# Kernel tuning notes

Measured on AMD Instinct MI355X. Metric: run time of the kernel, lower is better.

The kernel has to match this reference:

```python
import jax, jax.numpy as jnp
import numpy as np

# dims (match init_kwargs)
V = 100000   # vocab_size
E = 512      # embedding_dim
HID = 1024   # hidden_dim (bi-LSTM output size)
H = HID // 2 # per-direction LSTM hidden
T = 32       # num_of_tag
S = 8192     # sequence length
START, STOP = 30, 31
NEG = -10000.0


def setup_inputs() -> dict:
    key = jax.random.key(0)
    ks = jax.random.split(key, 11)
    n = lambda k, shape, s=0.1: jax.random.normal(k, shape, dtype=jnp.float32) * s
    trans = jax.random.normal(ks[9], (T, T), dtype=jnp.float32)
    trans = trans.at[:, START].set(NEG)   # nothing transitions INTO start
    trans = trans.at[STOP, :].set(NEG)    # nothing transitions OUT of stop
    return {
        "inputs": jax.random.randint(ks[0], (S,), 0, V, dtype=jnp.int32),
        "embed": n(ks[1], (V, E), 1.0),
        "W_ih_f": n(ks[2], (4 * H, E)),
        "W_hh_f": n(ks[3], (4 * H, H)),
        "b_f": n(ks[4], (4 * H,)),        # b_ih + b_hh fused
        "W_ih_b": n(ks[5], (4 * H, E)),
        "W_hh_b": n(ks[6], (4 * H, H)),
        "b_b": n(ks[7], (4 * H,)),
        "fc_W": n(ks[8], (T, HID)),
        "fc_b": jnp.zeros((T,), jnp.float32),
        "trans": trans,
    }


def _lstm_dir(x, W_ih, W_hh, b):
    """Single-direction LSTM, PyTorch gate order (i, f, g, o). x: [S, E] -> [S, H]."""
    xp = x @ W_ih.T + b  # [S, 4H], precomputed input projections

    def step(carry, xp_t):
        h, c = carry
        gates = xp_t + h @ W_hh.T
        i, f, g, o = jnp.split(gates, 4)
        i, f, o = jax.nn.sigmoid(i), jax.nn.sigmoid(f), jax.nn.sigmoid(o)
        g = jnp.tanh(g)
        c = f * c + i * g
        h = o * jnp.tanh(c)
        return (h, c), h

    init = (jnp.zeros((H,), x.dtype), jnp.zeros((H,), x.dtype))
    _, hs = jax.lax.scan(step, init, xp)
    return hs


def _viterbi(feats, trans):
    """feats: [S, T]. Vectorized Viterbi DP over the TxT transition matrix."""
    init = jnp.full((T,), NEG, feats.dtype).at[START].set(0.0)

    def step(prev, feat):
        scores = prev[:, None] + trans          # [prev_tag, next_tag]
        bp = jnp.argmax(scores, axis=0)         # best previous tag per next tag
        best = jnp.max(scores, axis=0) + feat   # original adds emit AFTER argmax
        return best, bp

    last_scores, bptrs = jax.lax.scan(step, init, feats)  # bptrs: [S, T]
    term = last_scores + trans[:, STOP]
    last = jnp.argmax(term)
    path_score = term[last]

    def back(tag, bp):
        prev = bp[tag]
        return prev, prev

    _, ys = jax.lax.scan(back, last, bptrs[::-1])
    # ys = [tag_{S-2}, ..., tag_0, START]; drop START, reverse, append final tag
    best_path = jnp.concatenate([ys[:-1][::-1], last[None]])  # [S]
    return path_score, best_path


def reference(inputs, embed, W_ih_f, W_hh_f, b_f, W_ih_b, W_hh_b, b_b, fc_W, fc_b, trans):
    x = embed[inputs]                                   # [S, E]
    h_f = _lstm_dir(x, W_ih_f, W_hh_f, b_f)             # [S, H]
    h_b = _lstm_dir(x[::-1], W_ih_b, W_hh_b, b_b)[::-1] # [S, H]
    lstm_out = jnp.concatenate([h_f, h_b], axis=-1)     # [S, HID]
    # dropout is identity at inference
    feats = lstm_out @ fc_W.T + fc_b                    # [S, T]
    return _viterbi(feats, trans)
```

## Files before the change

### kernel.cpp

```cpp
#include <hip/hip_runtime.h>
#include <hip/hip_bf16.h>
#include <cmath>


#define S_LEN 8192
#define E_DIM 512
#define H_DIM 512
#define G4    2048
#define TAGS  32
#define NWG   32
#define START_TAG 30
#define STOP_TAG  31
#define NEGV  (-10000.0f)

typedef float fx4 __attribute__((ext_vector_type(4)));
typedef unsigned long long u64;

__global__ __launch_bounds__(256) void xp_gemm(
    const int* __restrict__ inputs, const float* __restrict__ embed,
    const float* __restrict__ Wf, const float* __restrict__ bf,
    const float* __restrict__ Wb, const float* __restrict__ bb,
    float* __restrict__ xp)
{
  const int dir = blockIdx.z;
  const float* Wt = dir ? Wb : Wf;
  const float* bs = dir ? bb : bf;
  float* out = xp + (size_t)dir * S_LEN * G4;
  const int n0 = blockIdx.x * 64, m0 = blockIdx.y * 64;

  __shared__ float As[32][68];
  __shared__ float Bs[32][68];
  __shared__ int toks[64];

  const int tid = threadIdx.x;
  if (tid < 64) {
    int m = m0 + tid;
    toks[tid] = inputs[dir ? (S_LEN - 1 - m) : m];
  }
  __syncthreads();

  const int r  = tid >> 2;
  const int kq = (tid & 3) * 8;
  const int tm = tid >> 4;
  const int tn = tid & 15;

  float acc[4][4] = {};
  for (int k0 = 0; k0 < E_DIM; k0 += 32) {
    const float* ap = embed + (size_t)toks[r] * E_DIM + k0 + kq;
    fx4 a0 = *(const fx4*)ap;
    fx4 a1 = *(const fx4*)(ap + 4);
    const float* bpt = Wt + (size_t)(n0 + r) * E_DIM + k0 + kq;
    fx4 b0 = *(const fx4*)bpt;
    fx4 b1 = *(const fx4*)(bpt + 4);
    __syncthreads();
    As[kq+0][r]=a0.x; As[kq+1][r]=a0.y; As[kq+2][r]=a0.z; As[kq+3][r]=a0.w;
    As[kq+4][r]=a1.x; As[kq+5][r]=a1.y; As[kq+6][r]=a1.z; As[kq+7][r]=a1.w;
    Bs[kq+0][r]=b0.x; Bs[kq+1][r]=b0.y; Bs[kq+2][r]=b0.z; Bs[kq+3][r]=b0.w;
    Bs[kq+4][r]=b1.x; Bs[kq+5][r]=b1.y; Bs[kq+6][r]=b1.z; Bs[kq+7][r]=b1.w;
    __syncthreads();
    #pragma unroll
    for (int k = 0; k < 32; ++k) {
      fx4 av = *(const fx4*)&As[k][tm*4];
      fx4 bv = *(const fx4*)&Bs[k][tn*4];
      acc[0][0]=fmaf(av.x,bv.x,acc[0][0]); acc[0][1]=fmaf(av.x,bv.y,acc[0][1]);
      acc[0][2]=fmaf(av.x,bv.z,acc[0][2]); acc[0][3]=fmaf(av.x,bv.w,acc[0][3]);
      acc[1][0]=fmaf(av.y,bv.x,acc[1][0]); acc[1][1]=fmaf(av.y,bv.y,acc[1][1]);
      acc[1][2]=fmaf(av.y,bv.z,acc[1][2]); acc[1][3]=fmaf(av.y,bv.w,acc[1][3]);
      acc[2][0]=fmaf(av.z,bv.x,acc[2][0]); acc[2][1]=fmaf(av.z,bv.y,acc[2][1]);
      acc[2][2]=fmaf(av.z,bv.z,acc[2][2]); acc[2][3]=fmaf(av.z,bv.w,acc[2][3]);
      acc[3][0]=fmaf(av.w,bv.x,acc[3][0]); acc[3][1]=fmaf(av.w,bv.y,acc[3][1]);
      acc[3][2]=fmaf(av.w,bv.z,acc[3][2]); acc[3][3]=fmaf(av.w,bv.w,acc[3][3]);
    }
  }
  const int gn = n0 + tn*4;
  fx4 bias = *(const fx4*)&bs[gn];
  #pragma unroll
  for (int i = 0; i < 4; ++i) {
    fx4 res;
    res.x = acc[i][0] + bias.x; res.y = acc[i][1] + bias.y;
    res.z = acc[i][2] + bias.z; res.w = acc[i][3] + bias.w;
    *(fx4*)&out[(size_t)(m0 + tm*4 + i) * G4 + gn] = res;
  }
}

__global__ __launch_bounds__(256, 1) void lstm_seq(
    const float* __restrict__ Whh_f, const float* __restrict__ Whh_b,
    const float* __restrict__ xp, float* __restrict__ h_hist,
    u64* __restrict__ ring)
{
  const int bid = blockIdx.x;
  const int dir = bid >> 5, j = bid & 31;
  const float* Whh = dir ? Whh_b : Whh_f;
  const float* xpd = xp + (size_t)dir * S_LEN * G4;
  float* hh = h_hist + (size_t)dir * S_LEN * H_DIM;
  u64* rg = ring + (size_t)dir * 2 * H_DIM;

  const int tid  = threadIdx.x;
  const int lane = tid & 63;
  const int wid  = tid >> 6;
  const int gate = lane >> 4;
  const int mm   = lane & 15;
  const int grow = gate * 512 + j * 16 + mm;

  fx4 wreg[32];
  {
    const fx4* wp = (const fx4*)(Whh + (size_t)grow * H_DIM + wid * 128);
    #pragma unroll
    for (int k = 0; k < 32; ++k) wreg[k] = wp[k];
  }

  __shared__ __align__(16) float hq[4][128];
  __shared__ float partial[2][4][64];
  u64* my_ring0 = rg + (size_t)wid * 128 + lane * 2;

  float c_reg = 0.f;

  for (int t = 0; t < S_LEN; ++t) {
    const int tb = t & 1;
    float xpv = 0.f;
    if (wid == 0) xpv = xpd[(size_t)t * G4 + grow];

    fx4 accv = {0.f, 0.f, 0.f, 0.f};
    if (t > 0) {
      u64* rp = rg + (size_t)((t - 1) & 1) * H_DIM + wid * 128 + lane * 2;
      const unsigned want = (unsigned)t;
      u64 p0 = __hip_atomic_load(rp + 0, __ATOMIC_RELAXED, __HIP_MEMORY_SCOPE_AGENT);
      u64 p1 = __hip_atomic_load(rp + 1, __ATOMIC_RELAXED, __HIP_MEMORY_SCOPE_AGENT);
      while ((unsigned)(p0 >> 32) < want || (unsigned)(p1 >> 32) < want) {
        p0 = __hip_atomic_load(rp + 0, __ATOMIC_RELAXED, __HIP_MEMORY_SCOPE_AGENT);
        p1 = __hip_atomic_load(rp + 1, __ATOMIC_RELAXED, __HIP_MEMORY_SCOPE_AGENT);
      }
      union { unsigned u; float f; } v0, v1;
      v0.u = (unsigned)p0; v1.u = (unsigned)p1;
      hq[wid][lane * 2]     = v0.f;
      hq[wid][lane * 2 + 1] = v1.f;
      asm volatile("s_waitcnt lgkmcnt(0)" ::: "memory");
      __builtin_amdgcn_sched_barrier(0);

      const fx4* hv4 = (const fx4*)&hq[wid][0];
      #pragma unroll
      for (int k = 0; k < 32; ++k) {
        fx4 hv = hv4[k];
        accv.x = fmaf(wreg[k].x, hv.x, accv.x);
        accv.y = fmaf(wreg[k].y, hv.y, accv.y);
        accv.z = fmaf(wreg[k].z, hv.z, accv.z);
        accv.w = fmaf(wreg[k].w, hv.w, accv.w);
      }
    }
    partial[tb][wid][lane] = (accv.x + accv.y) + (accv.z + accv.w);
    __syncthreads();

    if (wid == 0) {
      float g = partial[tb][0][lane] + partial[tb][1][lane]
              + partial[tb][2][lane] + partial[tb][3][lane] + xpv;
      float act = (gate == 2) ? tanhf(g) : 1.f / (1.f + expf(-g));
      float fv = __shfl(act, mm + 16);
      float gv = __shfl(act, mm + 32);
      float ov = __shfl(act, mm + 48);
      if (lane < 16) {
        float cval = fv * c_reg + act * gv;
        c_reg = cval;
        float hval = ov * tanhf(cval);
        hh[(size_t)t * H_DIM + j * 16 + lane] = hval;
        union { float f; unsigned u; } hb; hb.f = hval;
        u64 pkt = ((u64)(unsigned)(t + 1) << 32) | hb.u;
        __hip_atomic_store(rg + (size_t)tb * H_DIM + j * 16 + lane, pkt,
                           __ATOMIC_RELAXED, __HIP_MEMORY_SCOPE_AGENT);
      }
    }
  }
  (void)my_ring0;
}

__global__ __launch_bounds__(256) void fc_feats(
    const float* __restrict__ h_hist, const float* __restrict__ fcW,
    const float* __restrict__ fcb, float* __restrict__ feats)
{
  const int s = blockIdx.x;
  const int tid = threadIdx.x;
  __shared__ __align__(16) float hcat[1024];
  __shared__ float red[8][32];
  const float* hf = h_hist + (size_t)s * H_DIM;
  const float* hb = h_hist + (size_t)S_LEN * H_DIM + (size_t)(S_LEN - 1 - s) * H_DIM;
  hcat[tid]       = hf[tid];
  hcat[256 + tid] = hf[256 + tid];
  hcat[512 + tid] = hb[tid];
  hcat[768 + tid] = hb[256 + tid];
  __syncthreads();
  const int jj = tid & 31, part = tid >> 5;
  const float* wr = fcW + (size_t)jj * 1024 + part * 128;
  float a = 0.f;
  #pragma unroll
  for (int k = 0; k < 128; k += 4) {
    fx4 wv = *(const fx4*)(wr + k);
    a = fmaf(wv.x, hcat[part*128 + k + 0], a);
    a = fmaf(wv.y, hcat[part*128 + k + 1], a);
    a = fmaf(wv.z, hcat[part*128 + k + 2], a);
    a = fmaf(wv.w, hcat[part*128 + k + 3], a);
  }
  red[part][jj] = a;
  __syncthreads();
  if (tid < 32) {
    float sum = fcb[tid];
    #pragma unroll
    for (int p = 0; p < 8; ++p) sum += red[p][tid];
    feats[(size_t)s * TAGS + tid] = sum;
  }
}

__global__ __launch_bounds__(64) void viterbi(
    const float* __restrict__ feats, const float* __restrict__ trans,
    unsigned char* __restrict__ bpg, float* __restrict__ out)
{
  const int lane = threadIdx.x;
  const int j = lane & 31, ph = lane >> 5;
  float tc[16];
  #pragma unroll
  for (int p = 0; p < 16; ++p) tc[p] = trans[(ph*16 + p) * TAGS + j];

  __shared__ float prev[32];
  if (lane < 32) prev[lane] = (lane == START_TAG) ? 0.f : NEGV;
  __syncthreads();

  float feat = feats[j];
  for (int t = 0; t < S_LEN; ++t) {
    float featn = (t + 1 < S_LEN) ? feats[(size_t)(t + 1) * TAGS + j] : 0.f;
    float best = -3.4e38f; int bpi = 0;
    #pragma unroll
    for (int p = 0; p < 16; ++p) {
      float sc = prev[ph*16 + p] + tc[p];
      if (sc > best) { best = sc; bpi = ph*16 + p; }
    }
    float ob  = __shfl_xor(best, 32);
    int   obp = __shfl_xor(bpi, 32);
    if (ob > best || (ob == best && obp < bpi)) { best = ob; bpi = obp; }
    __syncthreads();
    if (lane < 32) {
      bpg[(size_t)t * TAGS + j] = (unsigned char)bpi;
      prev[j] = best + feat;
    }
    __syncthreads();
    feat = featn;
  }

  float term = (lane < 32) ? prev[lane] + trans[lane * TAGS + STOP_TAG] : -3.4e38f;
  int idx = lane;
  #pragma unroll
  for (int off = 32; off >= 1; off >>= 1) {
    float os = __shfl_down(term, off);
    int   oi = __shfl_down(idx, off);
    if (os > term || (os == term && oi < idx)) { term = os; idx = oi; }
  }
  __shared__ int s_cur;
  if (lane == 0) {
    out[0] = term;
    out[1 + (S_LEN - 1)] = (float)idx;
    s_cur = idx;
  }

  __shared__ __align__(16) unsigned char bpc[1024 * TAGS];
  for (int ch = 7; ch >= 0; --ch) {
    __syncthreads();
    const int4* src = (const int4*)(bpg + (size_t)ch * 1024 * TAGS);
    int4* dst = (int4*)bpc;
    for (int i = lane; i < 2048; i += 64) dst[i] = src[i];
    __syncthreads();
    if (lane == 0) {
      int cur = s_cur;
      const int tlo = ch * 1024;
      for (int tt = 1023; tt >= 0; --tt) {
        int t = tlo + tt;
        if (t == 0) break;
        cur = bpc[tt * TAGS + cur];
        out[1 + (t - 1)] = (float)cur;
      }
      s_cur = cur;
    }
  }
}

extern "C" void kernel_launch(void* const* d_in, const int* in_sizes, int n_in,
                              void* d_out, int out_size, void* d_ws, size_t ws_size,
                              hipStream_t stream)
{
  (void)in_sizes; (void)n_in; (void)out_size; (void)ws_size;
  const int*   inputs = (const int*)d_in[0];
  const float* embed  = (const float*)d_in[1];
  const float* Wih_f  = (const float*)d_in[2];
  const float* Whh_f  = (const float*)d_in[3];
  const float* b_f    = (const float*)d_in[4];
  const float* Wih_b  = (const float*)d_in[5];
  const float* Whh_b  = (const float*)d_in[6];
  const float* b_b    = (const float*)d_in[7];
  const float* fcW    = (const float*)d_in[8];
  const float* fcb    = (const float*)d_in[9];
  const float* trans  = (const float*)d_in[10];
  float* out = (float*)d_out;

  float* ws     = (float*)d_ws;
  float* xp     = ws;
  float* h_hist = xp + (size_t)2 * S_LEN * G4;
  float* feats  = h_hist + (size_t)2 * S_LEN * H_DIM;
  unsigned char* bp = (unsigned char*)(feats + (size_t)S_LEN * TAGS);
  u64*   ring   = (u64*)(bp + (size_t)S_LEN * TAGS);

  hipMemsetAsync(ring, 0, 2 * 2 * H_DIM * sizeof(u64), stream);

  dim3 ggrid(G4 / 64, S_LEN / 64, 2);
  xp_gemm<<<ggrid, 256, 0, stream>>>(inputs, embed, Wih_f, b_f, Wih_b, b_b, xp);
  lstm_seq<<<64, 256, 0, stream>>>(Whh_f, Whh_b, xp, h_hist, ring);
  fc_feats<<<S_LEN, 256, 0, stream>>>(h_hist, fcW, fcb, feats);
  viterbi<<<1, 64, 0, stream>>>(feats, trans, bp, out);
}
```

Measured before the change: 17.15 ms.

## Cut LSTM and Viterbi recurrence latency with fast activations and prefetch

```diff
diff --git a/kernel.cpp b/kernel.cpp
--- a/kernel.cpp
+++ b/kernel.cpp
@@ -15,6 +15,24 @@
 
 typedef float fx4 __attribute__((ext_vector_type(4)));
 typedef unsigned long long u64;
+
+#if __has_builtin(__builtin_amdgcn_exp2f)
+__device__ __forceinline__ float fexp2(float x) { return __builtin_amdgcn_exp2f(x); }
+#else
+__device__ __forceinline__ float fexp2(float x) { return exp2f(x); }
+#endif
+#if __has_builtin(__builtin_amdgcn_rcpf)
+__device__ __forceinline__ float frcp(float x) { return __builtin_amdgcn_rcpf(x); }
+#else
+__device__ __forceinline__ float frcp(float x) { return 1.f / x; }
+#endif
+#define LOG2E 1.44269504088896340736f
+__device__ __forceinline__ float fsigmoid(float x) {
+  return frcp(1.f + fexp2(-LOG2E * x));
+}
+__device__ __forceinline__ float ftanh(float x) {
+  return fmaf(2.f, frcp(1.f + fexp2(-2.f * LOG2E * x)), -1.f);
+}
 
 __global__ __launch_bounds__(256) void xp_gemm(
     const int* __restrict__ inputs, const float* __restrict__ embed,
@@ -108,17 +126,20 @@
     #pragma unroll
     for (int k = 0; k < 32; ++k) wreg[k] = wp[k];
   }
+  #pragma unroll
+  for (int k = 0; k < 32; ++k) asm volatile("" : "+v"(wreg[k]));
 
   __shared__ __align__(16) float hq[4][128];
   __shared__ float partial[2][4][64];
-  u64* my_ring0 = rg + (size_t)wid * 128 + lane * 2;
 
   float c_reg = 0.f;
+  float xpv = 0.f;
+  if (wid == 0) xpv = xpd[grow];
 
   for (int t = 0; t < S_LEN; ++t) {
     const int tb = t & 1;
-    float xpv = 0.f;
-    if (wid == 0) xpv = xpd[(size_t)t * G4 + grow];
+    float xpn = 0.f;
+    if (wid == 0 && t + 1 < S_LEN) xpn = xpd[(size_t)(t + 1) * G4 + grow];
 
     fx4 accv = {0.f, 0.f, 0.f, 0.f};
     if (t > 0) {
@@ -126,14 +147,17 @@
       const unsigned want = (unsigned)t;
       u64 p0 = __hip_atomic_load(rp + 0, __ATOMIC_RELAXED, __HIP_MEMORY_SCOPE_AGENT);
       u64 p1 = __hip_atomic_load(rp + 1, __ATOMIC_RELAXED, __HIP_MEMORY_SCOPE_AGENT);
+      u64 q0 = __hip_atomic_load(rp + 0, __ATOMIC_RELAXED, __HIP_MEMORY_SCOPE_AGENT);
+      u64 q1 = __hip_atomic_load(rp + 1, __ATOMIC_RELAXED, __HIP_MEMORY_SCOPE_AGENT);
       while ((unsigned)(p0 >> 32) < want || (unsigned)(p1 >> 32) < want) {
-        p0 = __hip_atomic_load(rp + 0, __ATOMIC_RELAXED, __HIP_MEMORY_SCOPE_AGENT);
-        p1 = __hip_atomic_load(rp + 1, __ATOMIC_RELAXED, __HIP_MEMORY_SCOPE_AGENT);
+        p0 = q0; p1 = q1;
+        q0 = __hip_atomic_load(rp + 0, __ATOMIC_RELAXED, __HIP_MEMORY_SCOPE_AGENT);
+        q1 = __hip_atomic_load(rp + 1, __ATOMIC_RELAXED, __HIP_MEMORY_SCOPE_AGENT);
       }
       union { unsigned u; float f; } v0, v1;
       v0.u = (unsigned)p0; v1.u = (unsigned)p1;
-      hq[wid][lane * 2]     = v0.f;
-      hq[wid][lane * 2 + 1] = v1.f;
+      float2 hv2; hv2.x = v0.f; hv2.y = v1.f;
+      ((float2*)&hq[wid][0])[lane] = hv2;
       asm volatile("s_waitcnt lgkmcnt(0)" ::: "memory");
       __builtin_amdgcn_sched_barrier(0);
 
@@ -147,29 +171,30 @@
         accv.w = fmaf(wreg[k].w, hv.w, accv.w);
       }
     }
-    partial[tb][wid][lane] = (accv.x + accv.y) + (accv.z + accv.w);
+    float mypart = (accv.x + accv.y) + (accv.z + accv.w);
+    partial[tb][wid][lane] = mypart;
     __syncthreads();
 
     if (wid == 0) {
-      float g = partial[tb][0][lane] + partial[tb][1][lane]
+      float g = mypart + partial[tb][1][lane]
               + partial[tb][2][lane] + partial[tb][3][lane] + xpv;
-      float act = (gate == 2) ? tanhf(g) : 1.f / (1.f + expf(-g));
+      float act = (gate == 2) ? ftanh(g) : fsigmoid(g);
       float fv = __shfl(act, mm + 16);
       float gv = __shfl(act, mm + 32);
       float ov = __shfl(act, mm + 48);
       if (lane < 16) {
         float cval = fv * c_reg + act * gv;
         c_reg = cval;
-        float hval = ov * tanhf(cval);
-        hh[(size_t)t * H_DIM + j * 16 + lane] = hval;
+        float hval = ov * ftanh(cval);
         union { float f; unsigned u; } hb; hb.f = hval;
         u64 pkt = ((u64)(unsigned)(t + 1) << 32) | hb.u;
         __hip_atomic_store(rg + (size_t)tb * H_DIM + j * 16 + lane, pkt,
                            __ATOMIC_RELAXED, __HIP_MEMORY_SCOPE_AGENT);
+        hh[(size_t)t * H_DIM + j * 16 + lane] = hval;
       }
     }
-  }
-  (void)my_ring0;
+    xpv = xpn;
+  }
 }
 
 __global__ __launch_bounds__(256) void fc_feats(
@@ -218,32 +243,33 @@
   #pragma unroll
   for (int p = 0; p < 16; ++p) tc[p] = trans[(ph*16 + p) * TAGS + j];
 
-  __shared__ float prev[32];
-  if (lane < 32) prev[lane] = (lane == START_TAG) ? 0.f : NEGV;
+  __shared__ float prev[2][32];
+  if (lane < 32) prev[0][lane] = (lane == START_TAG) ? 0.f : NEGV;
   __syncthreads();
 
   float feat = feats[j];
   for (int t = 0; t < S_LEN; ++t) {
+    const int pb = t & 1;
     float featn = (t + 1 < S_LEN) ? feats[(size_t)(t + 1) * TAGS + j] : 0.f;
     float best = -3.4e38f; int bpi = 0;
     #pragma unroll
     for (int p = 0; p < 16; ++p) {
-      float sc = prev[ph*16 + p] + tc[p];
+      float sc = prev[pb][ph*16 + p] + tc[p];
       if (sc > best) { best = sc; bpi = ph*16 + p; }
     }
     float ob  = __shfl_xor(best, 32);
     int   obp = __shfl_xor(bpi, 32);
     if (ob > best || (ob == best && obp < bpi)) { best = ob; bpi = obp; }
-    __syncthreads();
     if (lane < 32) {
       bpg[(size_t)t * TAGS + j] = (unsigned char)bpi;
-      prev[j] = best + feat;
+      prev[pb ^ 1][j] = best + feat;
     }
     __syncthreads();
     feat = featn;
   }
 
-  float term = (lane < 32) ? prev[lane] + trans[lane * TAGS + STOP_TAG] : -3.4e38f;
+  float term = (lane < 32) ? prev[S_LEN & 1][lane] + trans[lane * TAGS + STOP_TAG]
+                           : -3.4e38f;
   int idx = lane;
   #pragma unroll
   for (int off = 32; off >= 1; off >>= 1) {
```

New measurement: 16.82 ms. About the same (-1.9%).
